# Optimization experiments

Measured on AMD Instinct MI355X. Metric: run time of the kernel, lower is better.

Reference implementation:

```python
import jax, jax.numpy as jnp
import numpy as np

NUM_HEADS = 16
EPS = 1e-6
CHUNK = 128  # chunk length for exact chunked-recurrent causal linear attention


def setup_inputs() -> dict:
    key = jax.random.key(0)
    ks = jax.random.split(key, 6)
    B, T, E = 4, 2048, 1024
    s = 0.02
    x = jax.random.normal(ks[0], (B, T, E), jnp.float32)
    Wq = jax.random.normal(ks[1], (E, E), jnp.float32) * s
    Wk = jax.random.normal(ks[2], (E, E), jnp.float32) * s
    Wv = jax.random.normal(ks[3], (E, E), jnp.float32) * s
    Wp = jax.random.normal(ks[4], (E, E), jnp.float32) * s
    bp = jnp.zeros((E,), jnp.float32)
    return {"x": x, "Wq": Wq, "Wk": Wk, "Wv": Wv, "Wp": Wp, "bp": bp}


def reference(x, Wq, Wk, Wv, Wp, bp):
    B, T, E = x.shape
    H = NUM_HEADS
    D = E // H
    N = T // CHUNK

    q = x @ Wq.T
    k = x @ Wk.T
    v = x @ Wv.T

    def split_heads(t):  # [B,T,E] -> [B,H,N,C,D]
        return t.reshape(B, T, H, D).transpose(0, 2, 1, 3).reshape(B, H, N, CHUNK, D)

    phi_q = jax.nn.elu(split_heads(q)) + 1.0
    phi_k = jax.nn.elu(split_heads(k)) + 1.0
    vh = split_heads(v)

    # per-chunk KV state and key-sum, then exclusive prefix over chunks
    kv = jnp.einsum('bhncd,bhnce->bhnde', phi_k, vh)        # [B,H,N,D,D]
    zk = phi_k.sum(axis=3)                                   # [B,H,N,D]
    S_prev = jnp.concatenate(
        [jnp.zeros_like(kv[:, :, :1]), jnp.cumsum(kv, axis=2)[:, :, :-1]], axis=2)
    Z_prev = jnp.concatenate(
        [jnp.zeros_like(zk[:, :, :1]), jnp.cumsum(zk, axis=2)[:, :, :-1]], axis=2)

    # intra-chunk causal part
    A = jnp.einsum('bhncd,bhnsd->bhncs', phi_q, phi_k)       # [B,H,N,C,C]
    mask = jnp.tril(jnp.ones((CHUNK, CHUNK), bool))
    A = jnp.where(mask, A, 0.0)

    num = (jnp.einsum('bhncs,bhnse->bhnce', A, vh)
           + jnp.einsum('bhncd,bhnde->bhnce', phi_q, S_prev))
    den = A.sum(-1) + jnp.einsum('bhncd,bhnd->bhnc', phi_q, Z_prev) + EPS
    y = num / den[..., None]                                  # [B,H,N,C,D]

    y = y.reshape(B, H, T, D).transpose(0, 2, 1, 3).reshape(B, T, E)
    return y @ Wp.T + bp
```

## Files before the change

### kernel.cpp

```cpp
#include <hip/hip_runtime.h>
#include <hip/hip_bf16.h>
#include <stdint.h>

#define T_LEN  2048
#define E_DIM  1024
#define BATCH  4
#define HEADS  16
#define HDIM   64
#define CHUNK_ 128
#define NCHUNK 16
#define EPS_   1e-6f

typedef __attribute__((ext_vector_type(8))) short bf16x8;
typedef __attribute__((ext_vector_type(4))) float f32x4;

__device__ __forceinline__ float b2f(__hip_bfloat16 h) { return __bfloat162float(h); }
__device__ __forceinline__ float bu2f(unsigned short u) {
  return __uint_as_float((unsigned)u << 16);
}
__device__ __forceinline__ unsigned short f2bu(float f) {
  __hip_bfloat16 h = __float2bfloat16(f);
  return *(unsigned short*)&h;
}
__device__ __forceinline__ void gld_lds16(const void* g, void* l) {
  __builtin_amdgcn_global_load_lds((const __attribute__((address_space(1))) void*)g,
                                   (__attribute__((address_space(3))) void*)l,
                                   16, 0, 0);
}

#define MFMA16(a, b, c) __builtin_amdgcn_mfma_f32_16x16x32_bf16((a), (b), (c), 0, 0, 0)

__global__ __launch_bounds__(256)
void cast5(const float* __restrict__ x,  const float* __restrict__ w0,
           const float* __restrict__ w1, const float* __restrict__ w2,
           const float* __restrict__ w3,
           __hip_bfloat16* __restrict__ xb,  __hip_bfloat16* __restrict__ w0b,
           __hip_bfloat16* __restrict__ w1b, __hip_bfloat16* __restrict__ w2b,
           __hip_bfloat16* __restrict__ w3b)
{
  const int b = blockIdx.x;
  const float* s;
  __hip_bfloat16* d;
  size_t off;
  if (b < 8192) { s = x; d = xb; off = (size_t)b * 1024; }
  else {
    const int i = (b - 8192) >> 10;
    const int r = (b - 8192) & 1023;
    s = (i == 0) ? w0 : (i == 1) ? w1 : (i == 2) ? w2 : w3;
    d = (i == 0) ? w0b : (i == 1) ? w1b : (i == 2) ? w2b : w3b;
    off = (size_t)r * 1024;
  }
  const int t = threadIdx.x;
  float4 v = *(const float4*)(s + off + (size_t)t * 4);
  ushort4 o;
  o.x = f2bu(v.x); o.y = f2bu(v.y); o.z = f2bu(v.z); o.w = f2bu(v.w);
  *(ushort4*)((unsigned short*)d + off + (size_t)t * 4) = o;
}

__global__ __launch_bounds__(512, 1)
void gemm_qkv_v2(const __hip_bfloat16* __restrict__ X,
                 const __hip_bfloat16* __restrict__ Wq,
                 const __hip_bfloat16* __restrict__ Wk,
                 const __hip_bfloat16* __restrict__ Wv,
                 __hip_bfloat16* __restrict__ qo,
                 __hip_bfloat16* __restrict__ ko,
                 __hip_bfloat16* __restrict__ vo)
{
  __shared__ __align__(16) unsigned short As[3][8192];
  __shared__ __align__(16) unsigned short Bs[3][16384];

  const int bm = blockIdx.x;
  const int byy = blockIdx.y;
  const int which = byy >> 2, bn = byy & 3;
  const __hip_bfloat16* Wsel = (which == 0) ? Wq : (which == 1) ? Wk : Wv;
  __hip_bfloat16* Cc = (which == 0) ? qo : (which == 1) ? ko : vo;
  const bool elu = (which < 2);

  const int t = threadIdx.x, lane = t & 63, wv = t >> 6;
  const int wm = (wv >> 2) * 64;
  const int wn = (wv & 3) * 64;

  const __hip_bfloat16* Xp = X + (size_t)(bm * 128) * 1024;
  const __hip_bfloat16* Wp = Wsel + (size_t)(bn * 256) * 1024;

  const int lo    = (lane & 15) * 128;
  const int lohi0 = lo + (((lane >> 4)    ) ^ (lane & 7)) * 16;
  const int lohi1 = lo + (((lane >> 4) | 4) ^ (lane & 7)) * 16;
  const int srow = lane >> 3;
  const int scg  = (lane & 7) ^ (lane >> 3);

  auto stA = [&](int buf, int k0) {
#pragma unroll
    for (int ci = 0; ci < 2; ++ci) {
      const int row0 = (wv * 2 + ci) * 8;
      gld_lds16(Xp + (size_t)(row0 + srow) * 1024 + k0 + scg * 8,
                (char*)&As[buf][0] + row0 * 128);
    }
  };
  auto stB0 = [&](int buf, int k0) {
#pragma unroll
    for (int ci = 0; ci < 2; ++ci) {
      const int row0 = (wv * 2 + ci) * 8;
      gld_lds16(Wp + (size_t)(row0 + srow) * 1024 + k0 + scg * 8,
                (char*)&Bs[buf][0] + row0 * 128);
    }
  };
  auto stB1 = [&](int buf, int k0) {
#pragma unroll
    for (int ci = 0; ci < 2; ++ci) {
      const int row0 = 128 + (wv * 2 + ci) * 8;
      gld_lds16(Wp + (size_t)(row0 + srow) * 1024 + k0 + scg * 8,
                (char*)&Bs[buf][0] + row0 * 128);
    }
  };
  auto rdA = [&](int buf, int half, bf16x8 (&d)[2][2]) {
#pragma unroll
    for (int m = 0; m < 2; ++m) {
      const int rb = wm + half * 32 + m * 16;
      d[m][0] = *(const bf16x8*)((const char*)&As[buf][0] + rb * 128 + lohi0);
      d[m][1] = *(const bf16x8*)((const char*)&As[buf][0] + rb * 128 + lohi1);
    }
  };
  auto rdB = [&](int buf, int half, bf16x8 (&d)[2][2]) {
#pragma unroll
    for (int n = 0; n < 2; ++n) {
      const int rb = wn + half * 32 + n * 16;
      d[n][0] = *(const bf16x8*)((const char*)&Bs[buf][0] + rb * 128 + lohi0);
      d[n][1] = *(const bf16x8*)((const char*)&Bs[buf][0] + rb * 128 + lohi1);
    }
  };

  f32x4 acc[4][4];
#pragma unroll
  for (int m = 0; m < 4; ++m)
#pragma unroll
    for (int n = 0; n < 4; ++n) acc[m][n] = (f32x4){0.f, 0.f, 0.f, 0.f};

  bf16x8 Aa01[2][2], Ab01[2][2], Aa23[2][2], Ab23[2][2];
  bf16x8 Ba01[2][2], Bb01[2][2], Ba23[2][2], Bb23[2][2];

  stA(0, 0);  stB0(0, 0);  stB1(0, 0);
  stA(1, 64); stB0(1, 64); stB1(1, 64);
  asm volatile("s_waitcnt vmcnt(6)" ::: "memory");
  __builtin_amdgcn_s_barrier();
  __builtin_amdgcn_sched_barrier(0);
  rdA(0, 0, Aa01); rdB(0, 0, Ab01); rdA(0, 1, Aa23); rdB(0, 1, Ab23);

  auto qstep = [&](int j, int c,
                   bf16x8 (&ca01)[2][2], bf16x8 (&cb01)[2][2],
                   bf16x8 (&ca23)[2][2], bf16x8 (&cb23)[2][2],
                   bf16x8 (&na01)[2][2], bf16x8 (&nb01)[2][2],
                   bf16x8 (&na23)[2][2], bf16x8 (&nb23)[2][2]) {
    const int stg  = (c + 2 >= 3) ? c - 1 : c + 2;
    const int nbuf = (c + 1 >= 3) ? 0 : c + 1;
    const int k0n  = (j + 2) * 64;
    const bool dost = (j < 14);

    __builtin_amdgcn_s_setprio(1);
#pragma unroll
    for (int m = 0; m < 2; ++m)
#pragma unroll
      for (int n = 0; n < 2; ++n) {
        acc[m][n] = MFMA16(ca01[m][0], cb01[n][0], acc[m][n]);
        acc[m][n] = MFMA16(ca01[m][1], cb01[n][1], acc[m][n]);
      }
    __builtin_amdgcn_s_setprio(0);
    if (dost) stA(stg, k0n);

    __builtin_amdgcn_s_setprio(1);
#pragma unroll
    for (int m = 0; m < 2; ++m)
#pragma unroll
      for (int n = 0; n < 2; ++n) {
        acc[m][2 + n] = MFMA16(ca01[m][0], cb23[n][0], acc[m][2 + n]);
        acc[m][2 + n] = MFMA16(ca01[m][1], cb23[n][1], acc[m][2 + n]);
      }
    __builtin_amdgcn_s_setprio(0);
    if (dost) stB0(stg, k0n);

    __builtin_amdgcn_s_setprio(1);
#pragma unroll
    for (int m = 0; m < 2; ++m)
#pragma unroll
      for (int n = 0; n < 2; ++n) {
        acc[2 + m][n] = MFMA16(ca23[m][0], cb01[n][0], acc[2 + m][n]);
        acc[2 + m][n] = MFMA16(ca23[m][1], cb01[n][1], acc[2 + m][n]);
      }
    __builtin_amdgcn_s_setprio(0);
    if (dost) stB1(stg, k0n);

    if (j == 14) asm volatile("s_waitcnt vmcnt(0)" ::: "memory");
    else         asm volatile("s_waitcnt vmcnt(6)" ::: "memory");
    __builtin_amdgcn_s_barrier();
    __builtin_amdgcn_sched_barrier(0);

    rdA(nbuf, 0, na01); rdB(nbuf, 0, nb01);

    __builtin_amdgcn_s_setprio(1);
#pragma unroll
    for (int m = 0; m < 2; ++m)
#pragma unroll
      for (int n = 0; n < 2; ++n) {
        acc[2 + m][2 + n] = MFMA16(ca23[m][0], cb23[n][0], acc[2 + m][2 + n]);
        acc[2 + m][2 + n] = MFMA16(ca23[m][1], cb23[n][1], acc[2 + m][2 + n]);
      }
    __builtin_amdgcn_s_setprio(0);

    rdA(nbuf, 1, na23); rdB(nbuf, 1, nb23);
  };

  int c = 0;
#pragma unroll 1
  for (int jj = 0; jj < 8; ++jj) {
    qstep(2 * jj, c, Aa01, Ab01, Aa23, Ab23, Ba01, Bb01, Ba23, Bb23);
    c = (c == 2) ? 0 : c + 1;
    qstep(2 * jj + 1, c, Ba01, Bb01, Ba23, Bb23, Aa01, Ab01, Aa23, Ab23);
    c = (c == 2) ? 0 : c + 1;
  }

  const int lm = lane & 15;
  const int r0 = (lane >> 4) * 4;
#pragma unroll
  for (int m = 0; m < 4; ++m) {
    const int row = bm * 128 + wm + m * 16 + r0;
#pragma unroll
    for (int n = 0; n < 4; ++n) {
      const int col = bn * 256 + wn + n * 16 + lm;
#pragma unroll
      for (int r = 0; r < 4; ++r) {
        float vv = acc[m][n][r];
        if (elu) vv = (vv > 0.f) ? (vv + 1.f) : __expf(vv);
        Cc[(size_t)(row + r) * 1024 + col] = __float2bfloat16(vv);
      }
    }
  }
}

__global__ __launch_bounds__(512, 1)
void gemm_out_v2(const __hip_bfloat16* __restrict__ X,
                 const __hip_bfloat16* __restrict__ W,
                 const float* __restrict__ bias,
                 float* __restrict__ C)
{
  __shared__ __align__(16) unsigned short As[3][8192];
  __shared__ __align__(16) unsigned short Bs[3][16384];

  const int bm = blockIdx.x;
  const int bn = blockIdx.y;

  const int t = threadIdx.x, lane = t & 63, wv = t >> 6;
  const int wm = (wv >> 2) * 64;
  const int wn = (wv & 3) * 64;

  const __hip_bfloat16* Xp = X + (size_t)(bm * 128) * 1024;
  const __hip_bfloat16* Wp = W + (size_t)(bn * 256) * 1024;

  const int lo    = (lane & 15) * 128;
  const int lohi0 = lo + (((lane >> 4)    ) ^ (lane & 7)) * 16;
  const int lohi1 = lo + (((lane >> 4) | 4) ^ (lane & 7)) * 16;
  const int srow = lane >> 3;
  const int scg  = (lane & 7) ^ (lane >> 3);

  auto stA = [&](int buf, int k0) {
#pragma unroll
    for (int ci = 0; ci < 2; ++ci) {
      const int row0 = (wv * 2 + ci) * 8;
      gld_lds16(Xp + (size_t)(row0 + srow) * 1024 + k0 + scg * 8,
                (char*)&As[buf][0] + row0 * 128);
    }
  };
  auto stB0 = [&](int buf, int k0) {
#pragma unroll
    for (int ci = 0; ci < 2; ++ci) {
      const int row0 = (wv * 2 + ci) * 8;
      gld_lds16(Wp + (size_t)(row0 + srow) * 1024 + k0 + scg * 8,
                (char*)&Bs[buf][0] + row0 * 128);
    }
  };
  auto stB1 = [&](int buf, int k0) {
#pragma unroll
    for (int ci = 0; ci < 2; ++ci) {
      const int row0 = 128 + (wv * 2 + ci) * 8;
      gld_lds16(Wp + (size_t)(row0 + srow) * 1024 + k0 + scg * 8,
                (char*)&Bs[buf][0] + row0 * 128);
    }
  };
  auto rdA = [&](int buf, int half, bf16x8 (&d)[2][2]) {
#pragma unroll
    for (int m = 0; m < 2; ++m) {
      const int rb = wm + half * 32 + m * 16;
      d[m][0] = *(const bf16x8*)((const char*)&As[buf][0] + rb * 128 + lohi0);
      d[m][1] = *(const bf16x8*)((const char*)&As[buf][0] + rb * 128 + lohi1);
    }
  };
  auto rdB = [&](int buf, int half, bf16x8 (&d)[2][2]) {
#pragma unroll
    for (int n = 0; n < 2; ++n) {
      const int rb = wn + half * 32 + n * 16;
      d[n][0] = *(const bf16x8*)((const char*)&Bs[buf][0] + rb * 128 + lohi0);
      d[n][1] = *(const bf16x8*)((const char*)&Bs[buf][0] + rb * 128 + lohi1);
    }
  };

  f32x4 acc[4][4];
#pragma unroll
  for (int m = 0; m < 4; ++m)
#pragma unroll
    for (int n = 0; n < 4; ++n) acc[m][n] = (f32x4){0.f, 0.f, 0.f, 0.f};

  bf16x8 Aa01[2][2], Ab01[2][2], Aa23[2][2], Ab23[2][2];
  bf16x8 Ba01[2][2], Bb01[2][2], Ba23[2][2], Bb23[2][2];

  stA(0, 0);  stB0(0, 0);  stB1(0, 0);
  stA(1, 64); stB0(1, 64); stB1(1, 64);
  asm volatile("s_waitcnt vmcnt(6)" ::: "memory");
  __builtin_amdgcn_s_barrier();
  __builtin_amdgcn_sched_barrier(0);
  rdA(0, 0, Aa01); rdB(0, 0, Ab01); rdA(0, 1, Aa23); rdB(0, 1, Ab23);

  auto qstep = [&](int j, int c,
                   bf16x8 (&ca01)[2][2], bf16x8 (&cb01)[2][2],
                   bf16x8 (&ca23)[2][2], bf16x8 (&cb23)[2][2],
                   bf16x8 (&na01)[2][2], bf16x8 (&nb01)[2][2],
                   bf16x8 (&na23)[2][2], bf16x8 (&nb23)[2][2]) {
    const int stg  = (c + 2 >= 3) ? c - 1 : c + 2;
    const int nbuf = (c + 1 >= 3) ? 0 : c + 1;
    const int k0n  = (j + 2) * 64;
    const bool dost = (j < 14);

    __builtin_amdgcn_s_setprio(1);
#pragma unroll
    for (int m = 0; m < 2; ++m)
#pragma unroll
      for (int n = 0; n < 2; ++n) {
        acc[m][n] = MFMA16(ca01[m][0], cb01[n][0], acc[m][n]);
        acc[m][n] = MFMA16(ca01[m][1], cb01[n][1], acc[m][n]);
      }
    __builtin_amdgcn_s_setprio(0);
    if (dost) stA(stg, k0n);

    __builtin_amdgcn_s_setprio(1);
#pragma unroll
    for (int m = 0; m < 2; ++m)
#pragma unroll
      for (int n = 0; n < 2; ++n) {
        acc[m][2 + n] = MFMA16(ca01[m][0], cb23[n][0], acc[m][2 + n]);
        acc[m][2 + n] = MFMA16(ca01[m][1], cb23[n][1], acc[m][2 + n]);
      }
    __builtin_amdgcn_s_setprio(0);
    if (dost) stB0(stg, k0n);

    __builtin_amdgcn_s_setprio(1);
#pragma unroll
    for (int m = 0; m < 2; ++m)
#pragma unroll
      for (int n = 0; n < 2; ++n) {
        acc[2 + m][n] = MFMA16(ca23[m][0], cb01[n][0], acc[2 + m][n]);
        acc[2 + m][n] = MFMA16(ca23[m][1], cb01[n][1], acc[2 + m][n]);
      }
    __builtin_amdgcn_s_setprio(0);
    if (dost) stB1(stg, k0n);

    if (j == 14) asm volatile("s_waitcnt vmcnt(0)" ::: "memory");
    else         asm volatile("s_waitcnt vmcnt(6)" ::: "memory");
    __builtin_amdgcn_s_barrier();
    __builtin_amdgcn_sched_barrier(0);

    rdA(nbuf, 0, na01); rdB(nbuf, 0, nb01);

    __builtin_amdgcn_s_setprio(1);
#pragma unroll
    for (int m = 0; m < 2; ++m)
#pragma unroll
      for (int n = 0; n < 2; ++n) {
        acc[2 + m][2 + n] = MFMA16(ca23[m][0], cb23[n][0], acc[2 + m][2 + n]);
        acc[2 + m][2 + n] = MFMA16(ca23[m][1], cb23[n][1], acc[2 + m][2 + n]);
      }
    __builtin_amdgcn_s_setprio(0);

    rdA(nbuf, 1, na23); rdB(nbuf, 1, nb23);
  };

  int c = 0;
#pragma unroll 1
  for (int jj = 0; jj < 8; ++jj) {
    qstep(2 * jj, c, Aa01, Ab01, Aa23, Ab23, Ba01, Bb01, Ba23, Bb23);
    c = (c == 2) ? 0 : c + 1;
    qstep(2 * jj + 1, c, Ba01, Bb01, Ba23, Bb23, Aa01, Ab01, Aa23, Ab23);
    c = (c == 2) ? 0 : c + 1;
  }

  const int lm = lane & 15;
  const int r0 = (lane >> 4) * 4;
#pragma unroll
  for (int m = 0; m < 4; ++m) {
    const int row = bm * 128 + wm + m * 16 + r0;
#pragma unroll
    for (int n = 0; n < 4; ++n) {
      const int col = bn * 256 + wn + n * 16 + lm;
      const float bv = bias[col];
#pragma unroll
      for (int r = 0; r < 4; ++r)
        C[(size_t)(row + r) * 1024 + col] = acc[m][n][r] + bv;
    }
  }
}

__global__ __launch_bounds__(256)
void chunk_kv(const __hip_bfloat16* __restrict__ Kp,
              const __hip_bfloat16* __restrict__ Vp,
              float* __restrict__ kvout, float* __restrict__ zkout,
              unsigned short* __restrict__ vimg)
{
  const int bid = blockIdx.x;
  const int n = bid & 15, h = (bid >> 4) & 15, b = bid >> 8;
  __shared__ __align__(16) __hip_bfloat16 ks[CHUNK_ * HDIM];
  __shared__ __align__(16) __hip_bfloat16 vs[CHUNK_ * HDIM];
  const size_t base = ((size_t)(b * T_LEN + n * CHUNK_)) * E_DIM + h * HDIM;
  const int t = threadIdx.x;
  for (int i = t; i < CHUNK_ * 8; i += 256) {
    int r = i >> 3, c = (i & 7) << 3;
    *(uint4*)&ks[r * HDIM + c] = *(const uint4*)(Kp + base + (size_t)r * E_DIM + c);
    *(uint4*)&vs[r * HDIM + c] = *(const uint4*)(Vp + base + (size_t)r * E_DIM + c);
  }
  __syncthreads();
  const int d0 = (t >> 4) << 2, e0 = (t & 15) << 2;
  const unsigned short* ksu = (const unsigned short*)ks;
  const unsigned short* vsu0 = (const unsigned short*)vs;
  float acc[4][4] = {{0.f}};
  float z[4] = {0.f, 0.f, 0.f, 0.f};
  for (int c = 0; c < CHUNK_; ++c) {
    ushort4 kq = *(const ushort4*)(ksu + c * HDIM + d0);
    ushort4 vq = *(const ushort4*)(vsu0 + c * HDIM + e0);
    float kv4[4], vv4[4];
    kv4[0] = bu2f(kq.x); kv4[1] = bu2f(kq.y); kv4[2] = bu2f(kq.z); kv4[3] = bu2f(kq.w);
    vv4[0] = bu2f(vq.x); vv4[1] = bu2f(vq.y); vv4[2] = bu2f(vq.z); vv4[3] = bu2f(vq.w);
#pragma unroll
    for (int i = 0; i < 4; ++i) {
      z[i] += kv4[i];
#pragma unroll
      for (int j = 0; j < 4; ++j) acc[i][j] += kv4[i] * vv4[j];
    }
  }
  float* o = kvout + (size_t)bid * (HDIM * HDIM);
  const int dg = d0 >> 3, doff = d0 & 7;
#pragma unroll
  for (int i = 0; i < 4; ++i)
#pragma unroll
    for (int j = 0; j < 4; ++j)
      o[dg * 512 + (e0 + j) * 8 + doff + i] = acc[i][j];
  if (e0 == 0) {
#pragma unroll
    for (int i = 0; i < 4; ++i) zkout[(size_t)bid * HDIM + d0 + i] = z[i];
  }
  const unsigned short* vsu = (const unsigned short*)vs;
  unsigned short* vo = vimg + (size_t)bid * 8192;
  for (int slot = t; slot < 1024; slot += 256) {
    const int sg = slot >> 6, e = slot & 63;
    ushort4 lo, hi;
    lo.x = vsu[(sg * 8 + 0) * 64 + e]; lo.y = vsu[(sg * 8 + 1) * 64 + e];
    lo.z = vsu[(sg * 8 + 2) * 64 + e]; lo.w = vsu[(sg * 8 + 3) * 64 + e];
    hi.x = vsu[(sg * 8 + 4) * 64 + e]; hi.y = vsu[(sg * 8 + 5) * 64 + e];
    hi.z = vsu[(sg * 8 + 6) * 64 + e]; hi.w = vsu[(sg * 8 + 7) * 64 + e];
    *(ushort4*)&vo[slot * 8] = lo;
    *(ushort4*)&vo[slot * 8 + 4] = hi;
  }
}

__global__ __launch_bounds__(256)
void prefix_chunks(float* __restrict__ S, float* __restrict__ Z)
{
  const int bh = blockIdx.x >> 2, seg = blockIdx.x & 3;
  const int t = threadIdx.x;
  float* base = S + (size_t)bh * NCHUNK * (HDIM * HDIM) + seg * 1024 + t * 4;
  float4 v[NCHUNK];
#pragma unroll
  for (int n = 0; n < NCHUNK; ++n)
    v[n] = *(const float4*)(base + (size_t)n * (HDIM * HDIM));
  float4 run = {0.f, 0.f, 0.f, 0.f};
#pragma unroll
  for (int n = 0; n < NCHUNK; ++n) {
    *(float4*)(base + (size_t)n * (HDIM * HDIM)) = run;
    run.x += v[n].x; run.y += v[n].y; run.z += v[n].z; run.w += v[n].w;
  }
  if (seg == 0 && t < 16) {
    float* zb = Z + (size_t)bh * NCHUNK * HDIM + t * 4;
    float4 zv[NCHUNK];
#pragma unroll
    for (int n = 0; n < NCHUNK; ++n) zv[n] = *(const float4*)(zb + n * HDIM);
    float4 zr = {0.f, 0.f, 0.f, 0.f};
#pragma unroll
    for (int n = 0; n < NCHUNK; ++n) {
      *(float4*)(zb + n * HDIM) = zr;
      zr.x += zv[n].x; zr.y += zv[n].y; zr.z += zv[n].z; zr.w += zv[n].w;
    }
  }
}

#define PW_STRIDE 136

__global__ __launch_bounds__(256, 3)
void chunk_attn(const __hip_bfloat16* __restrict__ Qp,
                const __hip_bfloat16* __restrict__ Kp,
                const unsigned short* __restrict__ vimg,
                const float* __restrict__ Simg,
                const float* __restrict__ Zp,
                __hip_bfloat16* __restrict__ Yp)
{
  __shared__ __align__(16) unsigned short VL[8192];
  __shared__ __align__(16) unsigned short SL[4096];
  __shared__ __align__(16) unsigned short PL[4 * 16 * PW_STRIDE];

  const int bid = blockIdx.x;
  const int n = bid & 15, h = (bid >> 4) & 15, b = bid >> 8;
  const int tokbase = b * T_LEN + n * CHUNK_;
  const size_t gbase = (size_t)tokbase * E_DIM + h * HDIM;
  const int t = threadIdx.x, lane = t & 63, wv = t >> 6;
  const int lm = lane & 15, kg = lane >> 4;

#pragma unroll
  for (int i = 0; i < 4; ++i) {
    const int j = wv * 4 + i;
    gld_lds16(vimg + (size_t)bid * 8192 + (size_t)(j * 64 + lane) * 8,
              (char*)VL + j * 1024);
  }
#pragma unroll
  for (int i = 0; i < 4; ++i) {
    const int idx = i * 1024 + t * 4;
    float4 s4 = *(const float4*)(Simg + (size_t)bid * 4096 + idx);
    ushort4 o;
    o.x = f2bu(s4.x); o.y = f2bu(s4.y); o.z = f2bu(s4.z); o.w = f2bu(s4.w);
    *(ushort4*)&SL[idx] = o;
  }

  const int mts[2] = { wv, 7 - wv };
  bf16x8 aq[2][2];
#pragma unroll
  for (int mi = 0; mi < 2; ++mi)
#pragma unroll
    for (int kh = 0; kh < 2; ++kh)
      aq[mi][kh] = *(const bf16x8*)(Qp + gbase +
                    (size_t)(mts[mi] * 16 + lm) * E_DIM + kh * 32 + kg * 8);
  bf16x8 zb[2];
#pragma unroll
  for (int kh = 0; kh < 2; ++kh) {
    float4 z0 = *(const float4*)(Zp + (size_t)bid * 64 + kh * 32 + kg * 8);
    float4 z1 = *(const float4*)(Zp + (size_t)bid * 64 + kh * 32 + kg * 8 + 4);
    zb[kh][0] = (short)f2bu(z0.x); zb[kh][1] = (short)f2bu(z0.y);
    zb[kh][2] = (short)f2bu(z0.z); zb[kh][3] = (short)f2bu(z0.w);
    zb[kh][4] = (short)f2bu(z1.x); zb[kh][5] = (short)f2bu(z1.y);
    zb[kh][6] = (short)f2bu(z1.z); zb[kh][7] = (short)f2bu(z1.w);
  }

  __syncthreads();

  f32x4 accn[2][4];
  f32x4 accden[2];
#pragma unroll
  for (int mi = 0; mi < 2; ++mi) {
    accden[mi] = (f32x4){EPS_, EPS_, EPS_, EPS_};
#pragma unroll
    for (int ne = 0; ne < 4; ++ne) accn[mi][ne] = (f32x4){0.f, 0.f, 0.f, 0.f};
  }

#pragma unroll
  for (int mi = 0; mi < 2; ++mi)
#pragma unroll
    for (int kh = 0; kh < 2; ++kh) {
      const bf16x8 a = aq[mi][kh];
      accden[mi] = MFMA16(a, zb[kh], accden[mi]);
#pragma unroll
      for (int ne = 0; ne < 4; ++ne) {
        bf16x8 bs = *(const bf16x8*)&SL[((kh * 4 + kg) * 64 + ne * 16 + lm) * 8];
        accn[mi][ne] = MFMA16(a, bs, accn[mi][ne]);
      }
    }

  unsigned short* Pw = PL + wv * 16 * PW_STRIDE;
  bf16x8 ones;
#pragma unroll
  for (int j = 0; j < 8; ++j) ones[j] = (short)0x3F80;

#pragma unroll
  for (int mi = 0; mi < 2; ++mi) {
    const int mt = mts[mi], m0 = mt * 16;
    for (int nt = 0; nt <= mt; ++nt) {
      f32x4 pt = (f32x4){0.f, 0.f, 0.f, 0.f};
#pragma unroll
      for (int kh = 0; kh < 2; ++kh) {
        bf16x8 ak = *(const bf16x8*)(Kp + gbase +
                     (size_t)(nt * 16 + lm) * E_DIM + kh * 32 + kg * 8);
        pt = MFMA16(ak, aq[mi][kh], pt);
      }
      unsigned short u[4];
#pragma unroll
      for (int r = 0; r < 4; ++r) {
        float v = pt[r];
        if (nt == mt) {
          v = ((kg * 4 + r) <= lm) ? v : 0.f;
        }
        u[r] = f2bu(v);
      }
      const int sidx = lm * PW_STRIDE + nt * 16 + kg * 4;
      *(unsigned*)&Pw[sidx]     = (unsigned)u[0] | ((unsigned)u[1] << 16);
      *(unsigned*)&Pw[sidx + 2] = (unsigned)u[2] | ((unsigned)u[3] << 16);
    }
    if ((mt & 1) == 0 && lane < 32) {
      const int m = lane >> 1, half = lane & 1;
      *(uint4*)&Pw[m * PW_STRIDE + (mt + 1) * 16 + half * 8] = (uint4){0u, 0u, 0u, 0u};
    }
    const int ktc = (mt + 2) >> 1;
    for (int kt = 0; kt < ktc; ++kt) {
      bf16x8 ap = *(const bf16x8*)&Pw[lm * PW_STRIDE + kt * 32 + kg * 8];
      accden[mi] = MFMA16(ap, ones, accden[mi]);
#pragma unroll
      for (int ne = 0; ne < 4; ++ne) {
        bf16x8 bv = *(const bf16x8*)&VL[((kt * 4 + kg) * 64 + ne * 16 + lm) * 8];
        accn[mi][ne] = MFMA16(ap, bv, accn[mi][ne]);
      }
    }
  }

#pragma unroll
  for (int mi = 0; mi < 2; ++mi) {
    const int m0 = mts[mi] * 16;
    float inv[4];
#pragma unroll
    for (int r = 0; r < 4; ++r) inv[r] = 1.f / accden[mi][r];
#pragma unroll
    for (int ne = 0; ne < 4; ++ne) {
      const int col = h * HDIM + ne * 16 + lm;
#pragma unroll
      for (int r = 0; r < 4; ++r) {
        const int row = tokbase + m0 + kg * 4 + r;
        Yp[(size_t)row * E_DIM + col] = __float2bfloat16(accn[mi][ne][r] * inv[r]);
      }
    }
  }
}

extern "C" void kernel_launch(void* const* d_in, const int* in_sizes, int n_in,
                              void* d_out, int out_size, void* d_ws, size_t ws_size,
                              hipStream_t stream)
{
  const float* x  = (const float*)d_in[0];
  const float* Wq = (const float*)d_in[1];
  const float* Wk = (const float*)d_in[2];
  const float* Wv = (const float*)d_in[3];
  const float* Wp = (const float*)d_in[4];
  const float* bp = (const float*)d_in[5];
  float* out = (float*)d_out;

  const size_t MT = (size_t)BATCH * T_LEN;
  char* w = (char*)d_ws;
  __hip_bfloat16* xb  = (__hip_bfloat16*)w; w += MT * E_DIM * sizeof(__hip_bfloat16);
  __hip_bfloat16* Wqb = (__hip_bfloat16*)w; w += (size_t)E_DIM * E_DIM * sizeof(__hip_bfloat16);
  __hip_bfloat16* Wkb = (__hip_bfloat16*)w; w += (size_t)E_DIM * E_DIM * sizeof(__hip_bfloat16);
  __hip_bfloat16* Wvb = (__hip_bfloat16*)w; w += (size_t)E_DIM * E_DIM * sizeof(__hip_bfloat16);
  __hip_bfloat16* Wpb = (__hip_bfloat16*)w; w += (size_t)E_DIM * E_DIM * sizeof(__hip_bfloat16);
  __hip_bfloat16* q = (__hip_bfloat16*)w; w += MT * E_DIM * sizeof(__hip_bfloat16);
  __hip_bfloat16* k = (__hip_bfloat16*)w; w += MT * E_DIM * sizeof(__hip_bfloat16);
  __hip_bfloat16* v = (__hip_bfloat16*)w; w += MT * E_DIM * sizeof(__hip_bfloat16);
  __hip_bfloat16* y = (__hip_bfloat16*)w; w += MT * E_DIM * sizeof(__hip_bfloat16);
  float* S = (float*)w; w += (size_t)BATCH * HEADS * NCHUNK * HDIM * HDIM * sizeof(float);
  float* Z = (float*)w; w += (size_t)BATCH * HEADS * NCHUNK * HDIM * sizeof(float);
  unsigned short* vimg = (unsigned short*)xb;

  cast5<<<8192 + 4096, 256, 0, stream>>>(x, Wq, Wk, Wv, Wp, xb, Wqb, Wkb, Wvb, Wpb);
  gemm_qkv_v2<<<dim3(64, 12), 512, 0, stream>>>(xb, Wqb, Wkb, Wvb, q, k, v);
  chunk_kv<<<BATCH * HEADS * NCHUNK, 256, 0, stream>>>(k, v, S, Z, vimg);
  prefix_chunks<<<BATCH * HEADS * 4, 256, 0, stream>>>(S, Z);
  chunk_attn<<<BATCH * HEADS * NCHUNK, 256, 0, stream>>>(q, k, vimg, S, Z, y);
  gemm_out_v2<<<dim3(64, 4), 512, 0, stream>>>(y, Wpb, bp, out);
}
```

Baseline: 234.3 us.

## Split fused QKV GEMM into three launches and swizzle attention P tile

The single 768-block QKV projection kernel becomes a generic per-matrix GEMM launched three times with 256 blocks each. In chunk_attn, the padded P scratch layout (stride 136) is replaced by an unpadded stride-128 layout with an XOR swizzle to avoid LDS bank conflicts. The smaller shared footprint lets launch bounds rise to 4 blocks per CU. Splitting the GEMM adds launch overhead and leaves each launch with fewer blocks than CUs, which can underfill the GPU.

```diff
diff --git a/kernel.cpp b/kernel.cpp
--- a/kernel.cpp
+++ b/kernel.cpp
@@ -58,30 +58,23 @@
 }
 
 __global__ __launch_bounds__(512, 1)
-void gemm_qkv_v2(const __hip_bfloat16* __restrict__ X,
-                 const __hip_bfloat16* __restrict__ Wq,
-                 const __hip_bfloat16* __restrict__ Wk,
-                 const __hip_bfloat16* __restrict__ Wv,
-                 __hip_bfloat16* __restrict__ qo,
-                 __hip_bfloat16* __restrict__ ko,
-                 __hip_bfloat16* __restrict__ vo)
+void gemm_proj(const __hip_bfloat16* __restrict__ X,
+               const __hip_bfloat16* __restrict__ W,
+               __hip_bfloat16* __restrict__ Cc,
+               int elu)
 {
   __shared__ __align__(16) unsigned short As[3][8192];
   __shared__ __align__(16) unsigned short Bs[3][16384];
 
   const int bm = blockIdx.x;
-  const int byy = blockIdx.y;
-  const int which = byy >> 2, bn = byy & 3;
-  const __hip_bfloat16* Wsel = (which == 0) ? Wq : (which == 1) ? Wk : Wv;
-  __hip_bfloat16* Cc = (which == 0) ? qo : (which == 1) ? ko : vo;
-  const bool elu = (which < 2);
+  const int bn = blockIdx.y;
 
   const int t = threadIdx.x, lane = t & 63, wv = t >> 6;
   const int wm = (wv >> 2) * 64;
   const int wn = (wv & 3) * 64;
 
   const __hip_bfloat16* Xp = X + (size_t)(bm * 128) * 1024;
-  const __hip_bfloat16* Wp = Wsel + (size_t)(bn * 256) * 1024;
+  const __hip_bfloat16* Wp = W + (size_t)(bn * 256) * 1024;
 
   const int lo    = (lane & 15) * 128;
   const int lohi0 = lo + (((lane >> 4)    ) ^ (lane & 7)) * 16;
@@ -497,9 +490,9 @@
   }
 }
 
-#define PW_STRIDE 136
-
-__global__ __launch_bounds__(256, 3)
+#define PW_STRIDE 128
+
+__global__ __launch_bounds__(256, 4)
 void chunk_attn(const __hip_bfloat16* __restrict__ Qp,
                 const __hip_bfloat16* __restrict__ Kp,
                 const unsigned short* __restrict__ vimg,
@@ -518,6 +511,10 @@
   const int t = threadIdx.x, lane = t & 63, wv = t >> 6;
   const int lm = lane & 15, kg = lane >> 4;
 
+  auto pswz = [](int m, int byteoff) {
+    return (m * 256 + byteoff) ^ ((m & 7) << 4);
+  };
+
 #pragma unroll
   for (int i = 0; i < 4; ++i) {
     const int j = wv * 4 + i;
@@ -577,6 +574,7 @@
     }
 
   unsigned short* Pw = PL + wv * 16 * PW_STRIDE;
+  char* Pwb = (char*)Pw;
   bf16x8 ones;
 #pragma unroll
   for (int j = 0; j < 8; ++j) ones[j] = (short)0x3F80;
@@ -601,17 +599,17 @@
         }
         u[r] = f2bu(v);
       }
-      const int sidx = lm * PW_STRIDE + nt * 16 + kg * 4;
-      *(unsigned*)&Pw[sidx]     = (unsigned)u[0] | ((unsigned)u[1] << 16);
-      *(unsigned*)&Pw[sidx + 2] = (unsigned)u[2] | ((unsigned)u[3] << 16);
+      const int pb = pswz(lm, nt * 32 + kg * 8);
+      *(unsigned*)(Pwb + pb)     = (unsigned)u[0] | ((unsigned)u[1] << 16);
+      *(unsigned*)(Pwb + pb + 4) = (unsigned)u[2] | ((unsigned)u[3] << 16);
     }
     if ((mt & 1) == 0 && lane < 32) {
       const int m = lane >> 1, half = lane & 1;
-      *(uint4*)&Pw[m * PW_STRIDE + (mt + 1) * 16 + half * 8] = (uint4){0u, 0u, 0u, 0u};
+      *(uint4*)(Pwb + pswz(m, (mt + 1) * 32 + half * 16)) = (uint4){0u, 0u, 0u, 0u};
     }
     const int ktc = (mt + 2) >> 1;
     for (int kt = 0; kt < ktc; ++kt) {
-      bf16x8 ap = *(const bf16x8*)&Pw[lm * PW_STRIDE + kt * 32 + kg * 8];
+      bf16x8 ap = *(const bf16x8*)(Pwb + pswz(lm, kt * 64 + kg * 16));
       accden[mi] = MFMA16(ap, ones, accden[mi]);
 #pragma unroll
       for (int ne = 0; ne < 4; ++ne) {
@@ -667,7 +665,9 @@
   unsigned short* vimg = (unsigned short*)xb;
 
   cast5<<<8192 + 4096, 256, 0, stream>>>(x, Wq, Wk, Wv, Wp, xb, Wqb, Wkb, Wvb, Wpb);
-  gemm_qkv_v2<<<dim3(64, 12), 512, 0, stream>>>(xb, Wqb, Wkb, Wvb, q, k, v);
+  gemm_proj<<<dim3(64, 4), 512, 0, stream>>>(xb, Wqb, q, 1);
+  gemm_proj<<<dim3(64, 4), 512, 0, stream>>>(xb, Wkb, k, 1);
+  gemm_proj<<<dim3(64, 4), 512, 0, stream>>>(xb, Wvb, v, 0);
   chunk_kv<<<BATCH * HEADS * NCHUNK, 256, 0, stream>>>(k, v, S, Z, vimg);
   prefix_chunks<<<BATCH * HEADS * 4, 256, 0, stream>>>(S, Z);
   chunk_attn<<<BATCH * HEADS * NCHUNK, 256, 0, stream>>>(q, k, vimg, S, Z, y);
```

Result: no change. 237.6 us (+1.4%).
